# Optimization experiments

Measured on AMD Instinct MI355X. Metric: run time of the kernel, lower is better.

The kernel has to match this reference:

```python
import jax, jax.numpy as jnp
import numpy as np

VOCAB, EMB, H, B, S = 32000, 512, 1024, 64, 128

def setup_inputs() -> dict:
    key = jax.random.key(0)
    ks = jax.random.split(key, 16)
    g = lambda k, shape, fan: jax.random.normal(k, shape, jnp.float32) * (1.0 / np.sqrt(fan))
    return {
        "dec_input": jax.random.randint(ks[0], (B, 1), 0, VOCAB),
        "hidden_state": jax.random.normal(ks[1], (B, H), jnp.float32),
        "enc_output": jax.random.normal(ks[2], (B, S, H), jnp.float32),
        "emb": g(ks[3], (VOCAB, EMB), EMB),
        "W1_k": g(ks[4], (H, H), H), "W1_b": jnp.zeros((H,), jnp.float32),
        "W2_k": g(ks[5], (H, H), H), "W2_b": jnp.zeros((H,), jnp.float32),
        "V_k": g(ks[6], (H, 1), H), "V_b": jnp.zeros((1,), jnp.float32),
        "gru_k": g(ks[7], (H + EMB, 3 * H), H + EMB),
        "gru_rk": g(ks[8], (H, 3 * H), H),
        "gru_b": jnp.zeros((2, 3 * H), jnp.float32),  # reset_after: input bias + recurrent bias
        "out_k": g(ks[9], (H, VOCAB), H), "out_b": jnp.zeros((VOCAB,), jnp.float32),
    }

def reference(dec_input, hidden_state, enc_output, emb, W1_k, W1_b, W2_k, W2_b,
              V_k, V_b, gru_k, gru_rk, gru_b, out_k, out_b):
    # Bahdanau additive attention
    # score: (B,S,1) = V(tanh(W1(enc) + W2(h)[:,None,:]))
    feat = jnp.tanh(jnp.einsum('bsh,hk->bsk', enc_output, W1_k) + W1_b
                    + (hidden_state @ W2_k + W2_b)[:, None, :])
    score = jnp.einsum('bsk,ko->bso', feat, V_k) + V_b          # (B,S,1)
    attention_weights = jax.nn.softmax(score, axis=1)            # (B,S,1)
    context = jnp.sum(attention_weights * enc_output, axis=1)    # (B,H)
    # embedding + concat (seq len 1 -> squeeze the time axis)
    x_emb = emb[dec_input[:, 0]]                                 # (B,EMB)
    x = jnp.concatenate([context, x_emb], axis=-1)               # (B,H+EMB)
    # GRU cell, one step, reset_after=True (Keras/CuDNN convention)
    xm = x @ gru_k + gru_b[0]                                    # (B,3H)
    hm = hidden_state @ gru_rk + gru_b[1]                        # (B,3H)
    Hd = hidden_state.shape[-1]
    xz, xr, xh = xm[:, :Hd], xm[:, Hd:2*Hd], xm[:, 2*Hd:]
    hz, hr, hh = hm[:, :Hd], hm[:, Hd:2*Hd], hm[:, 2*Hd:]
    z = jax.nn.sigmoid(xz + hz)
    r = jax.nn.sigmoid(xr + hr)
    h_cand = jnp.tanh(xh + r * hh)
    state = z * hidden_state + (1.0 - z) * h_cand                # (B,H)
    # seq len 1: GRU output == state; reshape(-1, H) is identity here
    probs = state @ out_k + out_b                                # (B,VOCAB)
    return probs, state, attention_weights
```

## Files before the change

kernel.cpp:

```cpp
#include <hip/hip_runtime.h>


#define B_ 64
#define S_ 128
#define H_ 1024
#define EMB_ 512
#define VOCAB_ 32000

typedef __attribute__((ext_vector_type(8))) short short8;
typedef __attribute__((ext_vector_type(4))) float f32x4;

__device__ __forceinline__ unsigned short f2bf_bits(float f) {
    unsigned int u = __float_as_uint(f);
    u += 0x7FFF + ((u >> 16) & 1);
    return (unsigned short)(u >> 16);
}
__device__ __forceinline__ float sigmoidf_(float x) { return 1.0f / (1.0f + expf(-x)); }
__device__ __forceinline__ int sw_(int r) { return (r ^ (r >> 2)) & 3; }
__device__ __forceinline__ int bf_(int n) { return (n ^ (n >> 2)) & 3; }
__device__ __forceinline__ float fc4_(const float4& v, int c) {
    return c == 0 ? v.x : c == 1 ? v.y : c == 2 ? v.z : v.w;
}

__device__ __forceinline__ short8 pack8_(float4 lo, float4 hi) {
    short8 s;
    s[0] = (short)f2bf_bits(lo.x);
    s[1] = (short)f2bf_bits(lo.y);
    s[2] = (short)f2bf_bits(lo.z);
    s[3] = (short)f2bf_bits(lo.w);
    s[4] = (short)f2bf_bits(hi.x);
    s[5] = (short)f2bf_bits(hi.y);
    s[6] = (short)f2bf_bits(hi.z);
    s[7] = (short)f2bf_bits(hi.w);
    return s;
}

template <int NF>
__device__ void mfma_gemm_tile(const float* __restrict__ A, int lda,
                               const float* __restrict__ W, int ldw,
                               int m_base, int n_base, int k0, int k1,
                               f32x4 (&acc)[4][NF]) {
    constexpr int NT = 64 * NF;
    constexpr int JOBS = (NF >= 2) ? NF / 2 : 1;
    __shared__ __attribute__((aligned(16))) unsigned short A_lds[2][64 * 32];
    __shared__ __attribute__((aligned(16))) unsigned short B_lds[2][NT * 32];
    const int tid = threadIdx.x;
    const int w = tid >> 6, lane = tid & 63, quad = lane >> 4, l15 = lane & 15;

    const f32x4 z = {0.0f, 0.0f, 0.0f, 0.0f};
#pragma unroll
    for (int mi = 0; mi < 4; ++mi)
#pragma unroll
        for (int ni = 0; ni < NF; ++ni) acc[mi][ni] = z;

    const int ar = tid >> 2, ac = tid & 3;
    const int aslot = ac ^ sw_(ar);
    int bk[JOBS], bn[JOBS];
    if constexpr (NF == 1) {
        bk[0] = 4 * (tid >> 5);
        bn[0] = 2 * (tid & 31);
    } else {
#pragma unroll
        for (int j = 0; j < JOBS; ++j) {
            int id = tid + 256 * j;
            bk[j] = 4 * (id / (16 * NF));
            bn[j] = 4 * (id % (16 * NF));
        }
    }

    float4 areg[2][2];
    float4 br4[2][JOBS][4];
    float2 br2[2][4];

#pragma unroll
    for (int s = 0; s < 2; ++s) {
        int kk = k0 + 32 * s;
        if (s == 0 || kk < k1) {
            const float* asrc = A + (size_t)(m_base + ar) * lda + kk + 8 * ac;
            areg[s][0] = *(const float4*)asrc;
            areg[s][1] = *(const float4*)(asrc + 4);
            if constexpr (NF == 1) {
                const float* bs = W + (size_t)(kk + bk[0]) * ldw + n_base + bn[0];
#pragma unroll
                for (int i = 0; i < 4; ++i)
                    br2[s][i] = *(const float2*)(bs + (size_t)i * ldw);
            } else {
#pragma unroll
                for (int j = 0; j < JOBS; ++j) {
                    const float* bs = W + (size_t)(kk + bk[j]) * ldw + n_base + bn[j];
#pragma unroll
                    for (int i = 0; i < 4; ++i)
                        br4[s][j][i] = *(const float4*)(bs + (size_t)i * ldw);
                }
            }
        }
    }

    int p = 0;
    for (int k = k0; k < k1; k += 64) {
#pragma unroll
        for (int s = 0; s < 2; ++s) {
            const int kk = k + 32 * s;
            *(short8*)&A_lds[p][ar * 32 + aslot * 8] = pack8_(areg[s][0], areg[s][1]);
            if constexpr (NF == 1) {
                const int kb = bk[0];
#pragma unroll
                for (int c = 0; c < 2; ++c) {
                    int n = bn[0] + c;
                    int si = n * 32 + ((((kb >> 3) ^ bf_(n)) << 3) + (kb & 7));
                    unsigned int lo, hi;
                    if (c == 0) {
                        lo = (unsigned)f2bf_bits(br2[s][0].x) |
                             ((unsigned)f2bf_bits(br2[s][1].x) << 16);
                        hi = (unsigned)f2bf_bits(br2[s][2].x) |
                             ((unsigned)f2bf_bits(br2[s][3].x) << 16);
                    } else {
                        lo = (unsigned)f2bf_bits(br2[s][0].y) |
                             ((unsigned)f2bf_bits(br2[s][1].y) << 16);
                        hi = (unsigned)f2bf_bits(br2[s][2].y) |
                             ((unsigned)f2bf_bits(br2[s][3].y) << 16);
                    }
                    uint2 wv;
                    wv.x = lo;
                    wv.y = hi;
                    *(uint2*)&B_lds[p][si] = wv;
                }
            } else {
#pragma unroll
                for (int j = 0; j < JOBS; ++j) {
                    const int kb = bk[j];
#pragma unroll
                    for (int c = 0; c < 4; ++c) {
                        int n = bn[j] + c;
                        int si = n * 32 + ((((kb >> 3) ^ bf_(n)) << 3) + (kb & 7));
                        unsigned int lo = (unsigned)f2bf_bits(fc4_(br4[s][j][0], c)) |
                                          ((unsigned)f2bf_bits(fc4_(br4[s][j][1], c)) << 16);
                        unsigned int hi = (unsigned)f2bf_bits(fc4_(br4[s][j][2], c)) |
                                          ((unsigned)f2bf_bits(fc4_(br4[s][j][3], c)) << 16);
                        uint2 wv;
                        wv.x = lo;
                        wv.y = hi;
                        *(uint2*)&B_lds[p][si] = wv;
                    }
                }
            }
            __syncthreads();
            const int kpre = kk + 64;
            if (kpre < k1) {
                const float* asrc = A + (size_t)(m_base + ar) * lda + kpre + 8 * ac;
                areg[s][0] = *(const float4*)asrc;
                areg[s][1] = *(const float4*)(asrc + 4);
                if constexpr (NF == 1) {
                    const float* bs = W + (size_t)(kpre + bk[0]) * ldw + n_base + bn[0];
#pragma unroll
                    for (int i = 0; i < 4; ++i)
                        br2[s][i] = *(const float2*)(bs + (size_t)i * ldw);
                } else {
#pragma unroll
                    for (int j = 0; j < JOBS; ++j) {
                        const float* bs =
                            W + (size_t)(kpre + bk[j]) * ldw + n_base + bn[j];
#pragma unroll
                        for (int i = 0; i < 4; ++i)
                            br4[s][j][i] = *(const float4*)(bs + (size_t)i * ldw);
                    }
                }
            }
            short8 bfrag[NF];
#pragma unroll
            for (int ni = 0; ni < NF; ++ni) {
                int nrel = w * 16 * NF + 16 * ni + l15;
                bfrag[ni] =
                    *(const short8*)&B_lds[p][nrel * 32 + ((quad ^ bf_(nrel)) << 3)];
            }
#pragma unroll
            for (int mi = 0; mi < 4; ++mi) {
                int r = 16 * mi + l15;
                short8 afrag =
                    *(const short8*)&A_lds[p][r * 32 + ((quad ^ sw_(r)) << 3)];
#pragma unroll
                for (int ni = 0; ni < NF; ++ni)
                    acc[mi][ni] = __builtin_amdgcn_mfma_f32_16x16x32_bf16(
                        afrag, bfrag[ni], acc[mi][ni], 0, 0, 0);
            }
            p ^= 1;
        }
    }
}

__global__ void init_bias4_kernel(float* __restrict__ hproj, const float* __restrict__ W2_b,
                                  float* __restrict__ hm, float* __restrict__ xm,
                                  const float* __restrict__ gru_b,
                                  float* __restrict__ score, const float* __restrict__ V_b) {
    int i = blockIdx.x * 256 + threadIdx.x;
    const int E0 = B_ * H_;
    const int E1 = E0 + B_ * 3 * H_;
    const int E2 = E1 + B_ * 3 * H_;
    const int E3 = E2 + B_ * S_;
    if (i < E0) {
        hproj[i] = W2_b[i & (H_ - 1)];
    } else if (i < E1) {
        int j = i - E0;
        hm[j] = gru_b[3 * H_ + j % (3 * H_)];
    } else if (i < E2) {
        int j = i - E1;
        xm[j] = gru_b[j % (3 * H_)];
    } else if (i < E3) {
        score[i - E2] = V_b[0];
    }
}

template <int NF>
__global__ __launch_bounds__(256) void gemm_mfma_atomic_kernel(
    const float* __restrict__ A, int lda, const float* __restrict__ W, int ldw,
    float* __restrict__ C, int kslice) {
    f32x4 acc[4][NF];
    const int n_base = blockIdx.x * 64 * NF;
    const int k0 = blockIdx.y * kslice;
    mfma_gemm_tile<NF>(A, lda, W, ldw, 0, n_base, k0, k0 + kslice, acc);
    const int tid = threadIdx.x, w = tid >> 6, lane = tid & 63;
    const int quad = lane >> 4, l15 = lane & 15;
#pragma unroll
    for (int mi = 0; mi < 4; ++mi)
#pragma unroll
        for (int ni = 0; ni < NF; ++ni) {
            int col = n_base + w * 16 * NF + 16 * ni + l15;
#pragma unroll
            for (int r = 0; r < 4; ++r) {
                int row = 16 * mi + quad * 4 + r;
                atomicAdd(&C[(size_t)row * ldw + col], acc[mi][ni][r]);
            }
        }
}

__global__ __launch_bounds__(256) void gemm_dual_kernel(
    const float* __restrict__ hidden, const float* __restrict__ W2_k,
    const float* __restrict__ gru_rk, float* __restrict__ hproj,
    float* __restrict__ hm, int kslice) {
    f32x4 acc[4][1];
    const int bx = blockIdx.x;
    const float* W;
    float* C;
    int ldw, n_base;
    if (bx < 16) {
        W = W2_k; C = hproj; ldw = H_; n_base = bx * 64;
    } else {
        W = gru_rk; C = hm; ldw = 3 * H_; n_base = (bx - 16) * 64;
    }
    const int k0 = blockIdx.y * kslice;
    mfma_gemm_tile<1>(hidden, H_, W, ldw, 0, n_base, k0, k0 + kslice, acc);
    const int tid = threadIdx.x, w = tid >> 6, lane = tid & 63;
    const int quad = lane >> 4, l15 = lane & 15;
#pragma unroll
    for (int mi = 0; mi < 4; ++mi) {
        int col = n_base + w * 16 + l15;
#pragma unroll
        for (int r = 0; r < 4; ++r) {
            int row = 16 * mi + quad * 4 + r;
            atomicAdd(&C[(size_t)row * ldw + col], acc[mi][0][r]);
        }
    }
}

__global__ __launch_bounds__(256) void score_mfma_kernel(
    const float* __restrict__ enc, const float* __restrict__ W1,
    const float* __restrict__ W1b, const float* __restrict__ Vk,
    const float* __restrict__ hproj, float* __restrict__ score) {
    f32x4 acc[4][4];
    const int n_base = blockIdx.x * 256;
    const int m_base = blockIdx.y * 64;
    const int b = m_base >> 7, s_base = m_base & 127;
    mfma_gemm_tile<4>(enc, H_, W1, H_, m_base, n_base, 0, H_, acc);

    const int tid = threadIdx.x, w = tid >> 6, lane = tid & 63;
    const int quad = lane >> 4, l15 = lane & 15;

    float rowpart[4][4];
#pragma unroll
    for (int mi = 0; mi < 4; ++mi)
#pragma unroll
        for (int r = 0; r < 4; ++r) rowpart[mi][r] = 0.0f;

#pragma unroll
    for (int ni = 0; ni < 4; ++ni) {
        int kcol = n_base + w * 64 + 16 * ni + l15;
        float add = W1b[kcol] + hproj[(size_t)b * H_ + kcol];
        float vv = Vk[kcol];
#pragma unroll
        for (int mi = 0; mi < 4; ++mi)
#pragma unroll
            for (int r = 0; r < 4; ++r)
                rowpart[mi][r] += tanhf(acc[mi][ni][r] + add) * vv;
    }
#pragma unroll
    for (int m = 1; m <= 8; m <<= 1)
#pragma unroll
        for (int mi = 0; mi < 4; ++mi)
#pragma unroll
            for (int r = 0; r < 4; ++r)
                rowpart[mi][r] += __shfl_xor(rowpart[mi][r], m, 64);
    if (l15 == 0) {
#pragma unroll
        for (int mi = 0; mi < 4; ++mi)
#pragma unroll
            for (int r = 0; r < 4; ++r)
                atomicAdd(&score[b * S_ + s_base + 16 * mi + quad * 4 + r],
                          rowpart[mi][r]);
    }
}

__global__ __launch_bounds__(256) void probs_mfma_kernel(
    const float* __restrict__ state, const float* __restrict__ out_k,
    const float* __restrict__ out_b, float* __restrict__ probs) {
    f32x4 acc[4][1];
    const int n_base = blockIdx.x * 64;
    mfma_gemm_tile<1>(state, H_, out_k, VOCAB_, 0, n_base, 0, H_, acc);
    const int tid = threadIdx.x, w = tid >> 6, lane = tid & 63;
    const int quad = lane >> 4, l15 = lane & 15;
    int col = n_base + w * 16 + l15;
    float bv = out_b[col];
#pragma unroll
    for (int mi = 0; mi < 4; ++mi) {
#pragma unroll
        for (int r = 0; r < 4; ++r) {
            int row = 16 * mi + quad * 4 + r;
            probs[(size_t)row * VOCAB_ + col] = acc[mi][0][r] + bv;
        }
    }
}

__global__ __launch_bounds__(256) void attn_ctx_kernel(
    const float* __restrict__ score, const float* __restrict__ enc,
    const float* __restrict__ emb, const int* __restrict__ dec,
    float* __restrict__ attn_out, float* __restrict__ xvec) {
    const int b = blockIdx.x >> 2, q = blockIdx.x & 3;
    const int t = threadIdx.x;
    __shared__ float red[128];
    __shared__ float aw[128];
    float v = 0.0f;
    if (t < 128) {
        v = score[b * S_ + t];
        red[t] = v;
    }
    __syncthreads();
    for (int str = 64; str > 0; str >>= 1) {
        if (t < str) red[t] = fmaxf(red[t], red[t + str]);
        __syncthreads();
    }
    float m = red[0];
    __syncthreads();
    float e = 0.0f;
    if (t < 128) {
        e = expf(v - m);
        red[t] = e;
    }
    __syncthreads();
    for (int str = 64; str > 0; str >>= 1) {
        if (t < str) red[t] += red[t + str];
        __syncthreads();
    }
    float inv = 1.0f / red[0];
    if (t < 128) aw[t] = e * inv;
    __syncthreads();

    const int col = q * 256 + t;
    const float* ebase = enc + (size_t)b * S_ * H_ + col;
    float a0 = 0.0f, a1 = 0.0f, a2 = 0.0f, a3 = 0.0f;
    for (int s = 0; s < S_; s += 4) {
        a0 += aw[s + 0] * ebase[(size_t)(s + 0) * H_];
        a1 += aw[s + 1] * ebase[(size_t)(s + 1) * H_];
        a2 += aw[s + 2] * ebase[(size_t)(s + 2) * H_];
        a3 += aw[s + 3] * ebase[(size_t)(s + 3) * H_];
    }
    xvec[(size_t)b * (H_ + EMB_) + col] = (a0 + a1) + (a2 + a3);

    if (q == 0 && t < 128) attn_out[b * S_ + t] = aw[t];
    if (q == 1) {
        int tok = dec[b];
        float* xb = xvec + (size_t)b * (H_ + EMB_) + H_;
        xb[t] = emb[(size_t)tok * EMB_ + t];
        xb[t + 256] = emb[(size_t)tok * EMB_ + t + 256];
    }
}

__global__ void gates_kernel(const float* __restrict__ xm, const float* __restrict__ hm,
                             const float* __restrict__ hidden,
                             float* __restrict__ state_out) {
    const int idx = blockIdx.x * 256 + threadIdx.x;
    const int b = idx >> 10, j = idx & (H_ - 1);
    const float* xmb = xm + (size_t)b * 3 * H_;
    const float* hmb = hm + (size_t)b * 3 * H_;
    float z = sigmoidf_(xmb[j] + hmb[j]);
    float r = sigmoidf_(xmb[H_ + j] + hmb[H_ + j]);
    float hc = tanhf(xmb[2 * H_ + j] + r * hmb[2 * H_ + j]);
    state_out[idx] = z * hidden[idx] + (1.0f - z) * hc;
}

extern "C" void kernel_launch(void* const* d_in, const int* in_sizes, int n_in,
                              void* d_out, int out_size, void* d_ws, size_t ws_size,
                              hipStream_t stream) {
    const int* dec_input = (const int*)d_in[0];
    const float* hidden = (const float*)d_in[1];
    const float* enc = (const float*)d_in[2];
    const float* emb = (const float*)d_in[3];
    const float* W1_k = (const float*)d_in[4];
    const float* W1_b = (const float*)d_in[5];
    const float* W2_k = (const float*)d_in[6];
    const float* W2_b = (const float*)d_in[7];
    const float* V_k = (const float*)d_in[8];
    const float* V_b = (const float*)d_in[9];
    const float* gru_k = (const float*)d_in[10];
    const float* gru_rk = (const float*)d_in[11];
    const float* gru_b = (const float*)d_in[12];
    const float* out_k = (const float*)d_in[13];
    const float* out_b = (const float*)d_in[14];

    float* out = (float*)d_out;
    float* probs_out = out;
    float* state_out = out + (size_t)B_ * VOCAB_;
    float* attn_out = state_out + (size_t)B_ * H_;

    float* hproj = probs_out;
    float* hm = hproj + B_ * H_;
    float* score = hm + B_ * 3 * H_;
    float* xvec = score + B_ * S_;
    float* xm = xvec + B_ * (H_ + EMB_);

    const int INIT_TOTAL = B_ * H_ + 2 * B_ * 3 * H_ + B_ * S_;
    init_bias4_kernel<<<(INIT_TOTAL + 255) / 256, 256, 0, stream>>>(
        hproj, W2_b, hm, xm, gru_b, score, V_b);

    gemm_dual_kernel<<<dim3(64, 8), 256, 0, stream>>>(hidden, W2_k, gru_rk, hproj,
                                                      hm, H_ / 8);
    score_mfma_kernel<<<dim3(4, 128), 256, 0, stream>>>(enc, W1_k, W1_b, V_k, hproj,
                                                        score);
    attn_ctx_kernel<<<B_ * 4, 256, 0, stream>>>(score, enc, emb, dec_input, attn_out,
                                                xvec);
    gemm_mfma_atomic_kernel<1><<<dim3(48, 8), 256, 0, stream>>>(xvec, H_ + EMB_, gru_k,
                                                                3 * H_, xm, (H_ + EMB_) / 8);
    gates_kernel<<<(B_ * H_) / 256, 256, 0, stream>>>(xm, hm, hidden, state_out);
    probs_mfma_kernel<<<dim3(VOCAB_ / 64), 256, 0, stream>>>(state_out, out_k, out_b,
                                                             probs_out);
}
```

Baseline: 368.4 us.

## Pre-transpose W1 to bf16 and restructure MFMA tile loaders

Adds a kernel that converts W1 to a transposed bf16 buffer each call, so the score GEMM can load its B operand as contiguous 16-byte vectors with no per-element conversion. The score grid becomes 1-D with a block-index swizzle meant to improve L2 reuse of the enc and W1 tiles. The single-column GEMM tile now loads B as scalar column reads with a 4-stage register prefetch, and the xm GEMM's k-split changes from 8 to 6 slices. The cost is an extra transpose launch and scratch traffic, plus strided scalar loads and higher register use in the other GEMMs.

```diff
diff --git a/kernel.cpp b/kernel.cpp
--- a/kernel.cpp
+++ b/kernel.cpp
@@ -17,10 +17,6 @@
 }
 __device__ __forceinline__ float sigmoidf_(float x) { return 1.0f / (1.0f + expf(-x)); }
 __device__ __forceinline__ int sw_(int r) { return (r ^ (r >> 2)) & 3; }
-__device__ __forceinline__ int bf_(int n) { return (n ^ (n >> 2)) & 3; }
-__device__ __forceinline__ float fc4_(const float4& v, int c) {
-    return c == 0 ? v.x : c == 1 ? v.y : c == 2 ? v.z : v.w;
-}
 
 __device__ __forceinline__ short8 pack8_(float4 lo, float4 hi) {
     short8 s;
@@ -35,151 +31,164 @@
     return s;
 }
 
-template <int NF>
-__device__ void mfma_gemm_tile(const float* __restrict__ A, int lda,
-                               const float* __restrict__ W, int ldw,
-                               int m_base, int n_base, int k0, int k1,
-                               f32x4 (&acc)[4][NF]) {
-    constexpr int NT = 64 * NF;
-    constexpr int JOBS = (NF >= 2) ? NF / 2 : 1;
+__global__ __launch_bounds__(256) void w1t_kernel(const float* __restrict__ W1,
+                                                  unsigned short* __restrict__ W1T) {
+    __shared__ unsigned short tile[64][72];
+    const int k0 = blockIdx.x * 64, n0 = blockIdx.y * 64;
+    const int t = threadIdx.x;
+    const int r = t >> 4, c4 = t & 15;
+#pragma unroll
+    for (int rr = 0; rr < 64; rr += 16) {
+        float4 v = *(const float4*)&W1[(size_t)(k0 + r + rr) * H_ + n0 + 4 * c4];
+        tile[4 * c4 + 0][r + rr] = f2bf_bits(v.x);
+        tile[4 * c4 + 1][r + rr] = f2bf_bits(v.y);
+        tile[4 * c4 + 2][r + rr] = f2bf_bits(v.z);
+        tile[4 * c4 + 3][r + rr] = f2bf_bits(v.w);
+    }
+    __syncthreads();
+    const int n = t >> 3, kc = t & 7;
+#pragma unroll
+    for (int pass = 0; pass < 2; ++pass) {
+        int nn = n + 32 * pass;
+        short8 s = *(const short8*)&tile[nn][8 * kc];
+        *(short8*)&W1T[(size_t)(n0 + nn) * H_ + k0 + 8 * kc] = s;
+    }
+}
+
+__device__ void mfma_gemm_tile1(const float* __restrict__ A, int lda,
+                                const float* __restrict__ W, int ldw,
+                                int n_base, int k0, int k1, f32x4 (&acc)[4]) {
     __shared__ __attribute__((aligned(16))) unsigned short A_lds[2][64 * 32];
-    __shared__ __attribute__((aligned(16))) unsigned short B_lds[2][NT * 32];
+    __shared__ __attribute__((aligned(16))) unsigned short B_lds[2][64 * 32];
     const int tid = threadIdx.x;
     const int w = tid >> 6, lane = tid & 63, quad = lane >> 4, l15 = lane & 15;
 
     const f32x4 z = {0.0f, 0.0f, 0.0f, 0.0f};
 #pragma unroll
-    for (int mi = 0; mi < 4; ++mi)
-#pragma unroll
-        for (int ni = 0; ni < NF; ++ni) acc[mi][ni] = z;
+    for (int mi = 0; mi < 4; ++mi) acc[mi] = z;
 
     const int ar = tid >> 2, ac = tid & 3;
     const int aslot = ac ^ sw_(ar);
-    int bk[JOBS], bn[JOBS];
-    if constexpr (NF == 1) {
-        bk[0] = 4 * (tid >> 5);
-        bn[0] = 2 * (tid & 31);
-    } else {
-#pragma unroll
-        for (int j = 0; j < JOBS; ++j) {
-            int id = tid + 256 * j;
-            bk[j] = 4 * (id / (16 * NF));
-            bn[j] = 4 * (id % (16 * NF));
-        }
-    }
-
-    float4 areg[2][2];
-    float4 br4[2][JOBS][4];
-    float2 br2[2][4];
-
-#pragma unroll
-    for (int s = 0; s < 2; ++s) {
-        int kk = k0 + 32 * s;
-        if (s == 0 || kk < k1) {
-            const float* asrc = A + (size_t)(m_base + ar) * lda + kk + 8 * ac;
-            areg[s][0] = *(const float4*)asrc;
-            areg[s][1] = *(const float4*)(asrc + 4);
-            if constexpr (NF == 1) {
-                const float* bs = W + (size_t)(kk + bk[0]) * ldw + n_base + bn[0];
-#pragma unroll
-                for (int i = 0; i < 4; ++i)
-                    br2[s][i] = *(const float2*)(bs + (size_t)i * ldw);
-            } else {
-#pragma unroll
-                for (int j = 0; j < JOBS; ++j) {
-                    const float* bs = W + (size_t)(kk + bk[j]) * ldw + n_base + bn[j];
-#pragma unroll
-                    for (int i = 0; i < 4; ++i)
-                        br4[s][j][i] = *(const float4*)(bs + (size_t)i * ldw);
-                }
-            }
-        }
+
+    float4 areg[4][2];
+    float breg[4][8];
+#pragma unroll
+    for (int s = 0; s < 4; ++s) {
+        const int kk = k0 + 32 * s;
+        const float* asrc = A + (size_t)ar * lda + kk + 8 * ac;
+        areg[s][0] = *(const float4*)asrc;
+        areg[s][1] = *(const float4*)(asrc + 4);
+        const float* bs = W + (size_t)(kk + 8 * ac) * ldw + n_base + ar;
+#pragma unroll
+        for (int j = 0; j < 8; ++j) breg[s][j] = bs[(size_t)j * ldw];
     }
 
     int p = 0;
-    for (int k = k0; k < k1; k += 64) {
-#pragma unroll
-        for (int s = 0; s < 2; ++s) {
-            const int kk = k + 32 * s;
+    for (int k = k0; k < k1; k += 128) {
+#pragma unroll
+        for (int s = 0; s < 4; ++s) {
             *(short8*)&A_lds[p][ar * 32 + aslot * 8] = pack8_(areg[s][0], areg[s][1]);
-            if constexpr (NF == 1) {
-                const int kb = bk[0];
-#pragma unroll
-                for (int c = 0; c < 2; ++c) {
-                    int n = bn[0] + c;
-                    int si = n * 32 + ((((kb >> 3) ^ bf_(n)) << 3) + (kb & 7));
-                    unsigned int lo, hi;
-                    if (c == 0) {
-                        lo = (unsigned)f2bf_bits(br2[s][0].x) |
-                             ((unsigned)f2bf_bits(br2[s][1].x) << 16);
-                        hi = (unsigned)f2bf_bits(br2[s][2].x) |
-                             ((unsigned)f2bf_bits(br2[s][3].x) << 16);
-                    } else {
-                        lo = (unsigned)f2bf_bits(br2[s][0].y) |
-                             ((unsigned)f2bf_bits(br2[s][1].y) << 16);
-                        hi = (unsigned)f2bf_bits(br2[s][2].y) |
-                             ((unsigned)f2bf_bits(br2[s][3].y) << 16);
-                    }
-                    uint2 wv;
-                    wv.x = lo;
-                    wv.y = hi;
-                    *(uint2*)&B_lds[p][si] = wv;
-                }
-            } else {
-#pragma unroll
-                for (int j = 0; j < JOBS; ++j) {
-                    const int kb = bk[j];
-#pragma unroll
-                    for (int c = 0; c < 4; ++c) {
-                        int n = bn[j] + c;
-                        int si = n * 32 + ((((kb >> 3) ^ bf_(n)) << 3) + (kb & 7));
-                        unsigned int lo = (unsigned)f2bf_bits(fc4_(br4[s][j][0], c)) |
-                                          ((unsigned)f2bf_bits(fc4_(br4[s][j][1], c)) << 16);
-                        unsigned int hi = (unsigned)f2bf_bits(fc4_(br4[s][j][2], c)) |
-                                          ((unsigned)f2bf_bits(fc4_(br4[s][j][3], c)) << 16);
-                        uint2 wv;
-                        wv.x = lo;
-                        wv.y = hi;
-                        *(uint2*)&B_lds[p][si] = wv;
-                    }
-                }
-            }
+            short8 bv;
+#pragma unroll
+            for (int j = 0; j < 8; ++j) bv[j] = (short)f2bf_bits(breg[s][j]);
+            *(short8*)&B_lds[p][ar * 32 + aslot * 8] = bv;
             __syncthreads();
-            const int kpre = kk + 64;
+            const int kpre = k + 32 * s + 128;
             if (kpre < k1) {
-                const float* asrc = A + (size_t)(m_base + ar) * lda + kpre + 8 * ac;
+                const float* asrc = A + (size_t)ar * lda + kpre + 8 * ac;
                 areg[s][0] = *(const float4*)asrc;
                 areg[s][1] = *(const float4*)(asrc + 4);
-                if constexpr (NF == 1) {
-                    const float* bs = W + (size_t)(kpre + bk[0]) * ldw + n_base + bn[0];
-#pragma unroll
-                    for (int i = 0; i < 4; ++i)
-                        br2[s][i] = *(const float2*)(bs + (size_t)i * ldw);
-                } else {
-#pragma unroll
-                    for (int j = 0; j < JOBS; ++j) {
-                        const float* bs =
-                            W + (size_t)(kpre + bk[j]) * ldw + n_base + bn[j];
-#pragma unroll
-                        for (int i = 0; i < 4; ++i)
-                            br4[s][j][i] = *(const float4*)(bs + (size_t)i * ldw);
-                    }
-                }
-            }
-            short8 bfrag[NF];
-#pragma unroll
-            for (int ni = 0; ni < NF; ++ni) {
-                int nrel = w * 16 * NF + 16 * ni + l15;
-                bfrag[ni] =
-                    *(const short8*)&B_lds[p][nrel * 32 + ((quad ^ bf_(nrel)) << 3)];
-            }
+                const float* bs = W + (size_t)(kpre + 8 * ac) * ldw + n_base + ar;
+#pragma unroll
+                for (int j = 0; j < 8; ++j) breg[s][j] = bs[(size_t)j * ldw];
+            }
+            const int nrel = w * 16 + l15;
+            short8 bfrag =
+                *(const short8*)&B_lds[p][nrel * 32 + ((quad ^ sw_(nrel)) << 3)];
 #pragma unroll
             for (int mi = 0; mi < 4; ++mi) {
                 int r = 16 * mi + l15;
                 short8 afrag =
                     *(const short8*)&A_lds[p][r * 32 + ((quad ^ sw_(r)) << 3)];
-#pragma unroll
-                for (int ni = 0; ni < NF; ++ni)
+                acc[mi] = __builtin_amdgcn_mfma_f32_16x16x32_bf16(afrag, bfrag,
+                                                                  acc[mi], 0, 0, 0);
+            }
+            p ^= 1;
+        }
+    }
+}
+
+__device__ void mfma_gemm_tile_bt4(const float* __restrict__ A, int lda,
+                                   const unsigned short* __restrict__ WT,
+                                   int n_base, f32x4 (&acc)[4][4]) {
+    __shared__ __attribute__((aligned(16))) unsigned short A_lds[2][64 * 32];
+    __shared__ __attribute__((aligned(16))) unsigned short B_lds[2][256 * 32];
+    const int tid = threadIdx.x;
+    const int w = tid >> 6, lane = tid & 63, quad = lane >> 4, l15 = lane & 15;
+
+    const f32x4 z = {0.0f, 0.0f, 0.0f, 0.0f};
+#pragma unroll
+    for (int mi = 0; mi < 4; ++mi)
+#pragma unroll
+        for (int ni = 0; ni < 4; ++ni) acc[mi][ni] = z;
+
+    const int ar = tid >> 2, ac = tid & 3;
+    const int aslot = ac ^ sw_(ar);
+    const int bn0 = tid >> 2, bc = tid & 3;
+
+    float4 areg[2][2];
+    short8 breg[2][4];
+#pragma unroll
+    for (int s = 0; s < 2; ++s) {
+        const int kk = 32 * s;
+        const float* asrc = A + (size_t)ar * lda + kk + 8 * ac;
+        areg[s][0] = *(const float4*)asrc;
+        areg[s][1] = *(const float4*)(asrc + 4);
+#pragma unroll
+        for (int i = 0; i < 4; ++i) {
+            int n = bn0 + 64 * i;
+            breg[s][i] =
+                *(const short8*)&WT[(size_t)(n_base + n) * H_ + kk + 8 * bc];
+        }
+    }
+
+    int p = 0;
+    for (int k = 0; k < 1024; k += 64) {
+#pragma unroll
+        for (int s = 0; s < 2; ++s) {
+            *(short8*)&A_lds[p][ar * 32 + aslot * 8] = pack8_(areg[s][0], areg[s][1]);
+#pragma unroll
+            for (int i = 0; i < 4; ++i) {
+                int n = bn0 + 64 * i;
+                *(short8*)&B_lds[p][n * 32 + ((bc ^ sw_(n)) << 3)] = breg[s][i];
+            }
+            __syncthreads();
+            const int kpre = k + 32 * s + 64;
+            if (kpre < 1024) {
+                const float* asrc = A + (size_t)ar * lda + kpre + 8 * ac;
+                areg[s][0] = *(const float4*)asrc;
+                areg[s][1] = *(const float4*)(asrc + 4);
+#pragma unroll
+                for (int i = 0; i < 4; ++i) {
+                    int n = bn0 + 64 * i;
+                    breg[s][i] =
+                        *(const short8*)&WT[(size_t)(n_base + n) * H_ + kpre + 8 * bc];
+                }
+            }
+            short8 bfrag[4];
+#pragma unroll
+            for (int ni = 0; ni < 4; ++ni) {
+                int nrel = w * 64 + 16 * ni + l15;
+                bfrag[ni] =
+                    *(const short8*)&B_lds[p][nrel * 32 + ((quad ^ sw_(nrel)) << 3)];
+            }
+#pragma unroll
+            for (int mi = 0; mi < 4; ++mi) {
+                int r = 16 * mi + l15;
+                short8 afrag =
+                    *(const short8*)&A_lds[p][r * 32 + ((quad ^ sw_(r)) << 3)];
+#pragma unroll
+                for (int ni = 0; ni < 4; ++ni)
                     acc[mi][ni] = __builtin_amdgcn_mfma_f32_16x16x32_bf16(
                         afrag, bfrag[ni], acc[mi][ni], 0, 0, 0);
             }
@@ -210,26 +219,22 @@
     }
 }
 
-template <int NF>
-__global__ __launch_bounds__(256) void gemm_mfma_atomic_kernel(
+__global__ __launch_bounds__(256) void gemm_xm_kernel(
     const float* __restrict__ A, int lda, const float* __restrict__ W, int ldw,
     float* __restrict__ C, int kslice) {
-    f32x4 acc[4][NF];
-    const int n_base = blockIdx.x * 64 * NF;
+    f32x4 acc[4];
+    const int n_base = blockIdx.x * 64;
     const int k0 = blockIdx.y * kslice;
-    mfma_gemm_tile<NF>(A, lda, W, ldw, 0, n_base, k0, k0 + kslice, acc);
+    mfma_gemm_tile1(A, lda, W, ldw, n_base, k0, k0 + kslice, acc);
     const int tid = threadIdx.x, w = tid >> 6, lane = tid & 63;
     const int quad = lane >> 4, l15 = lane & 15;
+    const int col = n_base + w * 16 + l15;
 #pragma unroll
     for (int mi = 0; mi < 4; ++mi)
 #pragma unroll
-        for (int ni = 0; ni < NF; ++ni) {
-            int col = n_base + w * 16 * NF + 16 * ni + l15;
-#pragma unroll
-            for (int r = 0; r < 4; ++r) {
-                int row = 16 * mi + quad * 4 + r;
-                atomicAdd(&C[(size_t)row * ldw + col], acc[mi][ni][r]);
-            }
+        for (int r = 0; r < 4; ++r) {
+            int row = 16 * mi + quad * 4 + r;
+            atomicAdd(&C[(size_t)row * ldw + col], acc[mi][r]);
         }
 }
 
@@ -237,7 +242,7 @@
     const float* __restrict__ hidden, const float* __restrict__ W2_k,
     const float* __restrict__ gru_rk, float* __restrict__ hproj,
     float* __restrict__ hm, int kslice) {
-    f32x4 acc[4][1];
+    f32x4 acc[4];
     const int bx = blockIdx.x;
     const float* W;
     float* C;
@@ -248,29 +253,30 @@
         W = gru_rk; C = hm; ldw = 3 * H_; n_base = (bx - 16) * 64;
     }
     const int k0 = blockIdx.y * kslice;
-    mfma_gemm_tile<1>(hidden, H_, W, ldw, 0, n_base, k0, k0 + kslice, acc);
+    mfma_gemm_tile1(hidden, H_, W, ldw, n_base, k0, k0 + kslice, acc);
     const int tid = threadIdx.x, w = tid >> 6, lane = tid & 63;
     const int quad = lane >> 4, l15 = lane & 15;
-#pragma unroll
-    for (int mi = 0; mi < 4; ++mi) {
-        int col = n_base + w * 16 + l15;
+    const int col = n_base + w * 16 + l15;
+#pragma unroll
+    for (int mi = 0; mi < 4; ++mi)
 #pragma unroll
         for (int r = 0; r < 4; ++r) {
             int row = 16 * mi + quad * 4 + r;
-            atomicAdd(&C[(size_t)row * ldw + col], acc[mi][0][r]);
-        }
-    }
+            atomicAdd(&C[(size_t)row * ldw + col], acc[mi][r]);
+        }
 }
 
 __global__ __launch_bounds__(256) void score_mfma_kernel(
-    const float* __restrict__ enc, const float* __restrict__ W1,
+    const float* __restrict__ enc, const unsigned short* __restrict__ W1T,
     const float* __restrict__ W1b, const float* __restrict__ Vk,
     const float* __restrict__ hproj, float* __restrict__ score) {
     f32x4 acc[4][4];
-    const int n_base = blockIdx.x * 256;
-    const int m_base = blockIdx.y * 64;
+    const int bid = blockIdx.x;
+    const int swz = (bid & 7) * 64 + (bid >> 3);
+    const int n_base = (swz & 3) * 256;
+    const int m_base = (swz >> 2) * 64;
     const int b = m_base >> 7, s_base = m_base & 127;
-    mfma_gemm_tile<4>(enc, H_, W1, H_, m_base, n_base, 0, H_, acc);
+    mfma_gemm_tile_bt4(enc + (size_t)m_base * H_, H_, W1T, n_base, acc);
 
     const int tid = threadIdx.x, w = tid >> 6, lane = tid & 63;
     const int quad = lane >> 4, l15 = lane & 15;
@@ -312,21 +318,20 @@
 __global__ __launch_bounds__(256) void probs_mfma_kernel(
     const float* __restrict__ state, const float* __restrict__ out_k,
     const float* __restrict__ out_b, float* __restrict__ probs) {
-    f32x4 acc[4][1];
+    f32x4 acc[4];
     const int n_base = blockIdx.x * 64;
-    mfma_gemm_tile<1>(state, H_, out_k, VOCAB_, 0, n_base, 0, H_, acc);
+    mfma_gemm_tile1(state, H_, out_k, VOCAB_, n_base, 0, H_, acc);
     const int tid = threadIdx.x, w = tid >> 6, lane = tid & 63;
     const int quad = lane >> 4, l15 = lane & 15;
-    int col = n_base + w * 16 + l15;
+    const int col = n_base + w * 16 + l15;
     float bv = out_b[col];
 #pragma unroll
-    for (int mi = 0; mi < 4; ++mi) {
+    for (int mi = 0; mi < 4; ++mi)
 #pragma unroll
         for (int r = 0; r < 4; ++r) {
             int row = 16 * mi + quad * 4 + r;
-            probs[(size_t)row * VOCAB_ + col] = acc[mi][0][r] + bv;
-        }
-    }
+            probs[(size_t)row * VOCAB_ + col] = acc[mi][r] + bv;
+        }
 }
 
 __global__ __launch_bounds__(256) void attn_ctx_kernel(
@@ -425,6 +430,9 @@
     float* score = hm + B_ * 3 * H_;
     float* xvec = score + B_ * S_;
     float* xm = xvec + B_ * (H_ + EMB_);
+    unsigned short* W1T = (unsigned short*)(xm + B_ * 3 * H_);
+
+    w1t_kernel<<<dim3(16, 16), 256, 0, stream>>>(W1_k, W1T);
 
     const int INIT_TOTAL = B_ * H_ + 2 * B_ * 3 * H_ + B_ * S_;
     init_bias4_kernel<<<(INIT_TOTAL + 255) / 256, 256, 0, stream>>>(
@@ -432,12 +440,11 @@
 
     gemm_dual_kernel<<<dim3(64, 8), 256, 0, stream>>>(hidden, W2_k, gru_rk, hproj,
                                                       hm, H_ / 8);
-    score_mfma_kernel<<<dim3(4, 128), 256, 0, stream>>>(enc, W1_k, W1_b, V_k, hproj,
-                                                        score);
+    score_mfma_kernel<<<512, 256, 0, stream>>>(enc, W1T, W1_b, V_k, hproj, score);
     attn_ctx_kernel<<<B_ * 4, 256, 0, stream>>>(score, enc, emb, dec_input, attn_out,
                                                 xvec);
-    gemm_mfma_atomic_kernel<1><<<dim3(48, 8), 256, 0, stream>>>(xvec, H_ + EMB_, gru_k,
-                                                                3 * H_, xm, (H_ + EMB_) / 8);
+    gemm_xm_kernel<<<dim3(48, 6), 256, 0, stream>>>(xvec, H_ + EMB_, gru_k, 3 * H_,
+                                                    xm, 256);
     gates_kernel<<<(B_ * H_) / 256, 256, 0, stream>>>(xm, hm, hidden, state_out);
     probs_mfma_kernel<<<dim3(VOCAB_ / 64), 256, 0, stream>>>(state_out, out_k, out_b,
                                                              probs_out);
```

New measurement: 368.0 us. Within noise of the previous version (-0.1%).
